# Kernel optimization log

Measured on AMD Instinct MI355X. Metric: run time of the kernel, lower is better.

## Reference

```python
import jax, jax.numpy as jnp
import numpy as np

# Topologies derived from init kwargs (inputs=64, outputs=64, state=512, net1 hidden=[512])
D = 64 + 64 + 512                      # 640 = concat(input, prev_output, state)
NET1 = [D, 512, 64]
NET3 = [D] + NET1 + [512]              # [640, 640, 512, 64, 512] (code reuses mutated net1 topo)
W_TOTAL = sum(NET3[j] * NET3[j + 1] for j in range(len(NET3) - 1))  # 802816
B_TOTAL = sum(NET3[1:])                # 1728
NET2 = [D] + NET1 + [W_TOTAL + B_TOTAL]  # [640, 640, 512, 64, 804544]


def _leaky(v):
    return jnp.where(v >= 0, v, 0.01 * v)


def setup_inputs() -> dict:
    key = jax.random.key(0)
    ks = jax.random.split(key, 16)
    inp = {
        "x": jax.random.normal(ks[0], (64,), jnp.float32),
        "prev_output": jnp.zeros((64,), jnp.float32),
        "state": jnp.zeros((512,), jnp.float32),
    }
    # net1 params (Linear stores W as [out, in])
    for i in range(len(NET1) - 1):
        inp[f"net1_w{i}"] = jax.random.normal(ks[1 + i], (NET1[i + 1], NET1[i]), jnp.float32) * 0.02
        inp[f"net1_b{i}"] = jnp.zeros((NET1[i + 1],), jnp.float32)
    # net2 params
    for i in range(len(NET2) - 1):
        inp[f"net2_w{i}"] = jax.random.normal(ks[5 + i], (NET2[i + 1], NET2[i]), jnp.float32) * 0.02
        inp[f"net2_b{i}"] = jnp.zeros((NET2[i + 1],), jnp.float32)
    return inp


def reference(x, prev_output, state,
              net1_w0, net1_b0, net1_w1, net1_b1,
              net2_w0, net2_b0, net2_w1, net2_b1,
              net2_w2, net2_b2, net2_w3, net2_b3):
    inpt = jnp.concatenate([x, prev_output, state])  # [640]

    # net2: hypernetwork producing flattened weights+biases for net3
    h = _leaky(net2_w0 @ inpt + net2_b0)
    h = _leaky(net2_w1 @ h + net2_b1)
    h = _leaky(net2_w2 @ h + net2_b2)
    x2 = jnp.tanh(net2_w3 @ h + net2_b3) * 0.5       # [W_TOTAL + B_TOTAL]
    weights = x2[:W_TOTAL]
    bias = x2[W_TOTAL:]

    # net3: apply generated weights sequentially (state update)
    x3 = inpt
    wi, bi = 0, 0
    for j in range(1, len(NET3)):
        out_d, in_d = NET3[j], NET3[j - 1]
        W = weights[wi:wi + out_d * in_d].reshape(out_d, in_d)
        b = bias[bi:bi + out_d]
        x3 = W @ x3 + b                               # 1D: x3 @ W.T == W @ x3
        if j != len(NET3) - 1:
            x3 = _leaky(x3)
        wi += out_d * in_d
        bi += out_d
    new_state = x3                                    # [512]

    # net1: output head
    h1 = _leaky(net1_w0 @ inpt + net1_b0)
    out = net1_w1 @ h1 + net1_b1                      # [64]

    # torch forward returns only `out`; new_state is the persistent buffer
    # update. We concatenate both so the full step math is observable.
    return jnp.concatenate([out, new_state])          # [576]
```

## Files before the change

kernel.cpp:

```cpp
#include <hip/hip_runtime.h>
#include <math.h>


#define WS_H0    0
#define WS_H1N1  640
#define WS_H1N2  1152
#define WS_H2    1664
#define WS_INPT  1728
#define WS_X3A   2368
#define WS_X3B   3008
#define WS_T     4096

#define N_ROWS   804544
#define N_WAVES  12571

typedef float vf4 __attribute__((ext_vector_type(4)));

__device__ __forceinline__ float leaky_f(float v) { return v >= 0.0f ? v : 0.01f * v; }

__device__ __forceinline__ float inpt_at(int i, const float* x, const float* po, const float* st) {
  return i < 64 ? x[i] : (i < 128 ? po[i - 64] : st[i - 128]);
}

__device__ __forceinline__ float half_tanh(float d) {
  float t = exp2f(d * 2.8853900817779268f);
  return 0.5f - __builtin_amdgcn_rcpf(t + 1.0f);
}

template <int IN>
__device__ __forceinline__ float row_dot(const float* __restrict__ wrow, const float* s_in, int lane) {
  const float4* w4 = (const float4*)wrow;
  const float4* s4 = (const float4*)s_in;
  float acc = 0.f;
  for (int j = lane; j < IN / 4; j += 64) {
    float4 a = w4[j];
    float4 b = s4[j];
    acc += a.x * b.x + a.y * b.y + a.z * b.z + a.w * b.w;
  }
  for (int off = 32; off; off >>= 1) acc += __shfl_xor(acc, off, 64);
  return acc;
}

__global__ __launch_bounds__(256) void k1a(const float* __restrict__ x, const float* __restrict__ po,
                                           const float* __restrict__ st,
                                           const float* __restrict__ w2_0, const float* __restrict__ b2_0,
                                           const float* __restrict__ w1_0, const float* __restrict__ b1_0,
                                           float* __restrict__ ws) {
  __shared__ __align__(16) float s_in[640];
  for (int i = threadIdx.x; i < 640; i += 256) {
    float v = inpt_at(i, x, po, st);
    s_in[i] = v;
    ws[WS_INPT + i] = v;
  }
  __syncthreads();
  int wave = threadIdx.x >> 6, lane = threadIdx.x & 63;
  int o = blockIdx.x * 4 + wave;
  const float* wrow;
  float bias;
  float* dst;
  if (o < 640) {
    wrow = w2_0 + (long long)o * 640; bias = b2_0[o]; dst = ws + WS_H0 + o;
  } else {
    int oo = o - 640;
    wrow = w1_0 + (long long)oo * 640; bias = b1_0[oo]; dst = ws + WS_H1N1 + oo;
  }
  float acc = row_dot<640>(wrow, s_in, lane);
  if (lane == 0) *dst = leaky_f(acc + bias);
}

__global__ __launch_bounds__(256) void k1b(const float* __restrict__ w2_1, const float* __restrict__ b2_1,
                                           const float* __restrict__ w1_1, const float* __restrict__ b1_1,
                                           float* __restrict__ ws, float* __restrict__ out) {
  __shared__ __align__(16) float s_h0[640];
  __shared__ __align__(16) float s_h1[512];
  for (int i = threadIdx.x; i < 640; i += 256) s_h0[i] = ws[WS_H0 + i];
  for (int i = threadIdx.x; i < 512; i += 256) s_h1[i] = ws[WS_H1N1 + i];
  __syncthreads();
  int wave = threadIdx.x >> 6, lane = threadIdx.x & 63;
  int o = blockIdx.x * 4 + wave;
  if (o < 512) {
    float acc = row_dot<640>(w2_1 + (long long)o * 640, s_h0, lane);
    if (lane == 0) ws[WS_H1N2 + o] = leaky_f(acc + b2_1[o]);
  } else {
    int oo = o - 512;
    float acc = row_dot<512>(w1_1 + (long long)oo * 512, s_h1, lane);
    if (lane == 0) out[oo] = acc + b1_1[oo];
  }
}

__global__ __launch_bounds__(256) void k1c(const float* __restrict__ w2_2, const float* __restrict__ b2_2,
                                           float* __restrict__ ws) {
  __shared__ __align__(16) float s_h[512];
  for (int i = threadIdx.x; i < 512; i += 256) s_h[i] = ws[WS_H1N2 + i];
  __syncthreads();
  int wave = threadIdx.x >> 6, lane = threadIdx.x & 63;
  int o = blockIdx.x * 4 + wave;
  float acc = row_dot<512>(w2_2 + (long long)o * 512, s_h, lane);
  if (lane == 0) ws[WS_H2 + o] = leaky_f(acc + b2_2[o]);
}

__global__ __launch_bounds__(256) void bigT(const float* __restrict__ w3, const float* __restrict__ b3,
                                            const float* __restrict__ h2p, float* __restrict__ t) {
  int wid = blockIdx.x * 4 + (threadIdx.x >> 6);
  if (wid >= N_WAVES) return;
  const int lane = threadIdx.x & 63;
  const int g = lane >> 4;
  const int gl = lane & 15;
  float4 hv = ((const float4*)h2p)[gl];
  const long long base = (long long)wid * 64;
  const int myrow = (gl << 2) + g;
  float bmine = b3[base + myrow];
  const vf4* wp = (const vf4*)(w3 + (base << 6));
  vf4 v[16];
#pragma unroll
  for (int q = 0; q < 16; q++) v[q] = __builtin_nontemporal_load(&wp[((q * 4 + g) << 4) + gl]);
  float myd = 0.f;
#pragma unroll
  for (int q = 0; q < 16; q++) {
    float d = v[q].x * hv.x + v[q].y * hv.y + v[q].z * hv.z + v[q].w * hv.w;
    d += __shfl_xor(d, 1, 64);
    d += __shfl_xor(d, 2, 64);
    d += __shfl_xor(d, 4, 64);
    d += __shfl_xor(d, 8, 64);
    if (gl == q) myd = d;
  }
  t[base + myrow] = half_tanh(myd + bmine);
}

template <int IN, bool LEAKY>
__global__ __launch_bounds__(256) void gml(const float* __restrict__ t, const float* __restrict__ x3in,
                                           float* __restrict__ x3out, long long wi, long long brow,
                                           int OUT) {
  __shared__ __align__(16) float s_in[IN];
  for (int i = threadIdx.x; i < IN; i += 256) s_in[i] = x3in[i];
  __syncthreads();
  int wave = threadIdx.x >> 6, lane = threadIdx.x & 63;
  int o = blockIdx.x * 4 + wave;
  if (o >= OUT) return;
  float acc = row_dot<IN>(t + wi + (long long)o * IN, s_in, lane);
  if (lane == 0) {
    acc += t[brow + o];
    x3out[o] = LEAKY ? leaky_f(acc) : acc;
  }
}

__global__ __launch_bounds__(1024) void gmlTail(const float* __restrict__ t, const float* __restrict__ ws,
                                                float* __restrict__ out) {
  __shared__ __align__(16) float s_b[512];
  __shared__ __align__(16) float s_c[64];
  const int tid = threadIdx.x;
  const int wave = tid >> 6, lane = tid & 63;
  for (int i = tid; i < 512; i += 1024) s_b[i] = ws[WS_X3B + i];
  __syncthreads();
#pragma unroll
  for (int r = 0; r < 4; r++) {
    int o = wave + r * 16;
    float acc = row_dot<512>(t + 737280 + (long long)o * 512, s_b, lane);
    if (lane == 0) s_c[o] = leaky_f(acc + t[803968 + o]);
  }
  __syncthreads();
  const int g = lane >> 4, gl = lane & 15;
  float4 xc4 = ((const float4*)s_c)[gl];
#pragma unroll
  for (int r = 0; r < 8; r++) {
    int o = r * 64 + wave * 4 + g;
    const float4* row = (const float4*)(t + 770048 + (long long)o * 64);
    float4 wv = row[gl];
    float a = wv.x * xc4.x + wv.y * xc4.y + wv.z * xc4.z + wv.w * xc4.w;
    a += __shfl_xor(a, 1, 64);
    a += __shfl_xor(a, 2, 64);
    a += __shfl_xor(a, 4, 64);
    a += __shfl_xor(a, 8, 64);
    if (gl == 0) out[64 + o] = a + t[804032 + o];
  }
}

extern "C" void kernel_launch(void* const* d_in, const int* in_sizes, int n_in,
                              void* d_out, int out_size, void* d_ws, size_t ws_size,
                              hipStream_t stream) {
  const float* x    = (const float*)d_in[0];
  const float* po   = (const float*)d_in[1];
  const float* st   = (const float*)d_in[2];
  const float* w1_0 = (const float*)d_in[3];
  const float* b1_0 = (const float*)d_in[4];
  const float* w1_1 = (const float*)d_in[5];
  const float* b1_1 = (const float*)d_in[6];
  const float* w2_0 = (const float*)d_in[7];
  const float* b2_0 = (const float*)d_in[8];
  const float* w2_1 = (const float*)d_in[9];
  const float* b2_1 = (const float*)d_in[10];
  const float* w2_2 = (const float*)d_in[11];
  const float* b2_2 = (const float*)d_in[12];
  const float* w3   = (const float*)d_in[13];
  const float* b3   = (const float*)d_in[14];
  float* ws  = (float*)d_ws;
  float* out = (float*)d_out;
  float* t   = ws + WS_T;

  k1a<<<288, 256, 0, stream>>>(x, po, st, w2_0, b2_0, w1_0, b1_0, ws);
  k1b<<<144, 256, 0, stream>>>(w2_1, b2_1, w1_1, b1_1, ws, out);
  k1c<<<16, 256, 0, stream>>>(w2_2, b2_2, ws);
  bigT<<<(N_WAVES + 3) / 4, 256, 0, stream>>>(w3, b3, ws + WS_H2, t);
  gml<640, true><<<160, 256, 0, stream>>>(t, ws + WS_INPT, ws + WS_X3A, 0LL, 802816LL, 640);
  gml<640, true><<<128, 256, 0, stream>>>(t, ws + WS_X3A, ws + WS_X3B, 409600LL, 803456LL, 512);
  gmlTail<<<1, 1024, 0, stream>>>(t, ws, out);
}
```

Measured before the change: 325.9 us.

## Fuse first generated layer into hypernetwork output kernel via partial dot products

The big weight-generating kernel now also multiplies each generated first-layer weight by the input vector and reduces per-wave partial sums into a workspace buffer. A new kernel sums the ten partials per row, applies bias and leaky, then computes the second generated layer. This drops one kernel launch and the re-read of the first layer's 409600 generated weights from memory. The cost is extra shuffle reductions and input loads in the first 6400 waves of the bandwidth-bound kernel, plus 64000 partial-sum writes.

```diff
diff --git a/kernel.cpp b/kernel.cpp
--- a/kernel.cpp
+++ b/kernel.cpp
@@ -10,6 +10,7 @@
 #define WS_X3A   2368
 #define WS_X3B   3008
 #define WS_T     4096
+#define WS_PART  808640
 
 #define N_ROWS   804544
 #define N_WAVES  12571
@@ -100,7 +101,8 @@
 }
 
 __global__ __launch_bounds__(256) void bigT(const float* __restrict__ w3, const float* __restrict__ b3,
-                                            const float* __restrict__ h2p, float* __restrict__ t) {
+                                            const float* __restrict__ h2p, float* __restrict__ t,
+                                            const float* __restrict__ inpt, float* __restrict__ part) {
   int wid = blockIdx.x * 4 + (threadIdx.x >> 6);
   if (wid >= N_WAVES) return;
   const int lane = threadIdx.x & 63;
@@ -124,24 +126,36 @@
     d += __shfl_xor(d, 8, 64);
     if (gl == q) myd = d;
   }
-  t[base + myrow] = half_tanh(myd + bmine);
-}
-
-template <int IN, bool LEAKY>
-__global__ __launch_bounds__(256) void gml(const float* __restrict__ t, const float* __restrict__ x3in,
-                                           float* __restrict__ x3out, long long wi, long long brow,
-                                           int OUT) {
-  __shared__ __align__(16) float s_in[IN];
-  for (int i = threadIdx.x; i < IN; i += 256) s_in[i] = x3in[i];
-  __syncthreads();
-  int wave = threadIdx.x >> 6, lane = threadIdx.x & 63;
-  int o = blockIdx.x * 4 + wave;
-  if (o >= OUT) return;
-  float acc = row_dot<IN>(t + wi + (long long)o * IN, s_in, lane);
-  if (lane == 0) {
-    acc += t[brow + o];
-    x3out[o] = LEAKY ? leaky_f(acc) : acc;
-  }
+  float tval = half_tanh(myd + bmine);
+  t[base + myrow] = tval;
+  if (wid < 6400) {
+    int o = wid / 10, chunk = wid - o * 10;
+    float p = tval * inpt[chunk * 64 + myrow];
+    p += __shfl_xor(p, 1, 64);
+    p += __shfl_xor(p, 2, 64);
+    p += __shfl_xor(p, 4, 64);
+    p += __shfl_xor(p, 8, 64);
+    p += __shfl_xor(p, 16, 64);
+    p += __shfl_xor(p, 32, 64);
+    if (lane == 0) part[o * 10 + chunk] = p;
+  }
+}
+
+__global__ __launch_bounds__(256) void gml2x(const float* __restrict__ t, const float* __restrict__ part,
+                                             float* __restrict__ x3b) {
+  __shared__ __align__(16) float s_in[640];
+  for (int o = threadIdx.x; o < 640; o += 256) {
+    const float* pp = part + o * 10;
+    float s = 0.f;
+#pragma unroll
+    for (int c = 0; c < 10; c++) s += pp[c];
+    s_in[o] = leaky_f(s + t[802816 + o]);
+  }
+  __syncthreads();
+  int wave = threadIdx.x >> 6, lane = threadIdx.x & 63;
+  int o = blockIdx.x * 4 + wave;
+  float acc = row_dot<640>(t + 409600 + (long long)o * 640, s_in, lane);
+  if (lane == 0) x3b[o] = leaky_f(acc + t[803456 + o]);
 }
 
 __global__ __launch_bounds__(1024) void gmlTail(const float* __restrict__ t, const float* __restrict__ ws,
@@ -200,8 +214,7 @@
   k1a<<<288, 256, 0, stream>>>(x, po, st, w2_0, b2_0, w1_0, b1_0, ws);
   k1b<<<144, 256, 0, stream>>>(w2_1, b2_1, w1_1, b1_1, ws, out);
   k1c<<<16, 256, 0, stream>>>(w2_2, b2_2, ws);
-  bigT<<<(N_WAVES + 3) / 4, 256, 0, stream>>>(w3, b3, ws + WS_H2, t);
-  gml<640, true><<<160, 256, 0, stream>>>(t, ws + WS_INPT, ws + WS_X3A, 0LL, 802816LL, 640);
-  gml<640, true><<<128, 256, 0, stream>>>(t, ws + WS_X3A, ws + WS_X3B, 409600LL, 803456LL, 512);
+  bigT<<<(N_WAVES + 3) / 4, 256, 0, stream>>>(w3, b3, ws + WS_H2, t, ws + WS_INPT, ws + WS_PART);
+  gml2x<<<128, 256, 0, stream>>>(t, ws + WS_PART, ws + WS_X3B);
   gmlTail<<<1, 1024, 0, stream>>>(t, ws, out);
 }
```

After: 324.9 us. Within noise of the previous version (-0.3%).
